# Kernel optimization log

Hardware: AMD Instinct MI355X
Metric: run time of the kernel (lower is better)

Reference implementation:

```python
import jax, jax.numpy as jnp
import numpy as np


def setup_inputs() -> dict:
    key = jax.random.key(0)
    ks = jax.random.split(key, 10)
    N, E, H, T = 50000, 800000, 128, 2
    inp = {
        "hv": jax.random.normal(ks[0], (N, H), jnp.float32),
        "he": jax.random.normal(ks[1], (E, H), jnp.float32),
        "src": jax.random.randint(ks[2], (E,), 0, N, jnp.int32),
        "dst": jax.random.randint(ks[3], (E,), 0, N, jnp.int32),
        "W_msg": jax.random.normal(ks[4], (T, 2 * H, 3 * H), jnp.float32) * 0.05,
        "b_msg": jnp.zeros((T, 2 * H), jnp.float32),
        "W_ih": jax.random.normal(ks[5], (T, 3 * H, 2 * H), jnp.float32) * 0.05,
        "W_hh": jax.random.normal(ks[6], (T, 3 * H, H), jnp.float32) * 0.05,
        "b_ih": jnp.zeros((T, 3 * H), jnp.float32),
        "b_hh": jnp.zeros((T, 3 * H), jnp.float32),
    }
    return inp


def reference(hv, he, src, dst, W_msg, b_msg, W_ih, W_hh, b_ih, b_hh):
    N = hv.shape[0]
    T = W_msg.shape[0]
    # In-degree for mean reduction (DGL mailbox mean). Zero-degree nodes get zero message parts.
    deg = jax.ops.segment_sum(jnp.ones(dst.shape, hv.dtype), dst, num_segments=N)
    safe_deg = jnp.maximum(deg, 1.0)[:, None]  # [N,1]
    # Edge features are constant across rounds -> precompute their per-node mean.
    mean_he = jax.ops.segment_sum(he, dst, num_segments=N) / safe_deg  # [N,H]
    for t in range(T):
        # mean over mailbox of concat([hv_dst, hv_src, he]) then Linear == Linear of means (affine).
        mean_hsrc = jax.ops.segment_sum(hv[src], dst, num_segments=N) / safe_deg  # [N,H]
        x = jnp.concatenate([hv, mean_hsrc, mean_he], axis=1)  # [N,3H]
        a = x @ W_msg[t].T + b_msg[t]  # [N,2H] node activation
        # torch GRUCell(a, hv)
        gi = a @ W_ih[t].T + b_ih[t]   # [N,3H]
        gh = hv @ W_hh[t].T + b_hh[t]  # [N,3H]
        i_r, i_z, i_n = jnp.split(gi, 3, axis=1)
        h_r, h_z, h_n = jnp.split(gh, 3, axis=1)
        r = jax.nn.sigmoid(i_r + h_r)
        z = jax.nn.sigmoid(i_z + h_z)
        n = jnp.tanh(i_n + r * h_n)
        hv = (1.0 - z) * n + z * hv
    return hv
```

## Files before the change

### kernel.cpp

```cpp
#include <hip/hip_runtime.h>
#include <hip/hip_bf16.h>

typedef __bf16 bf16x8 __attribute__((ext_vector_type(8)));
typedef __bf16 bf16x2 __attribute__((ext_vector_type(2)));
typedef float  f32x4  __attribute__((ext_vector_type(4)));

#define MFMA16(a,b,c) __builtin_amdgcn_mfma_f32_16x16x32_bf16((a),(b),(c),0,0,0)

__global__ void k_prepack_weights(const float* __restrict__ wmsg,
                                  const float* __restrict__ wih,
                                  const float* __restrict__ whh,
                                  __bf16* __restrict__ o_msg,
                                  __bf16* __restrict__ o_rz,
                                  __bf16* __restrict__ o_in,
                                  __bf16* __restrict__ o_hn) {
    const int C1 = 2 * 256 * 384;
    const int C2 = C1 + 2 * 256 * 384;
    const int C3 = C2 + 2 * 128 * 256;
    const int C4 = C3 + 2 * 128 * 128;
    int i = blockIdx.x * 256 + threadIdx.x;
    if (i >= C4) return;
    if (i < C1) {
        o_msg[i] = (__bf16)wmsg[i];
    } else if (i < C2) {
        int p = i - C1;
        int t = p / 98304, rem = p % 98304;
        int o = rem / 384, c = rem % 384;
        float v = (c < 128) ? whh[t * 49152 + o * 128 + c]
                            : wih[t * 98304 + o * 256 + (c - 128)];
        o_rz[p] = (__bf16)v;
    } else if (i < C3) {
        int p = i - C2;
        int t = p / 32768, rem = p % 32768;
        int j = rem / 256, k = rem % 256;
        o_in[p] = (__bf16)wih[t * 98304 + (256 + j) * 256 + k];
    } else {
        int p = i - C3;
        int t = p / 16384, rem = p % 16384;
        int j = rem / 128, k = rem % 128;
        o_hn[p] = (__bf16)whh[t * 49152 + (256 + j) * 128 + k];
    }
}

__global__ void k_convert_hv(const float* __restrict__ hv, __bf16* __restrict__ hv_bf,
                             int total8) {
    int i = blockIdx.x * 256 + threadIdx.x;
    if (i >= total8) return;
    const float4* p = (const float4*)(hv + (size_t)i * 8);
    float4 a = p[0], b = p[1];
    bf16x8 o;
    o[0] = (__bf16)a.x; o[1] = (__bf16)a.y; o[2] = (__bf16)a.z; o[3] = (__bf16)a.w;
    o[4] = (__bf16)b.x; o[5] = (__bf16)b.y; o[6] = (__bf16)b.z; o[7] = (__bf16)b.w;
    *(bf16x8*)(hv_bf + (size_t)i * 8) = o;
}

__global__ void k_deg(const int* __restrict__ dst, int* __restrict__ degi, int E) {
    int e = blockIdx.x * 256 + threadIdx.x;
    if (e < E) atomicAdd(&degi[dst[e]], 1);
}

__global__ void k_alloc(const int* __restrict__ degi, int* __restrict__ off,
                        int* __restrict__ cnt, int* __restrict__ counter, int N) {
    int i = blockIdx.x * 256 + threadIdx.x;
    int lane = (int)threadIdx.x & 63;
    int v = (i < N) ? degi[i] : 0;
    int incl = v;
    #pragma unroll
    for (int d = 1; d < 64; d <<= 1) {
        int t = __shfl_up(incl, d, 64);
        if (lane >= d) incl += t;
    }
    int base = 0;
    if (lane == 63) base = atomicAdd(counter, incl);
    base = __shfl(base, 63, 64);
    if (i < N) { off[i] = base + incl - v; cnt[i] = 0; }
}

__global__ void k_bucket(const int* __restrict__ src, const int* __restrict__ dst,
                         const int* __restrict__ off, int* __restrict__ cnt,
                         int2* __restrict__ pairs, int E) {
    int e = blockIdx.x * 256 + threadIdx.x;
    if (e < E) {
        int d = dst[e];
        int p = off[d] + atomicAdd(&cnt[d], 1);
        pairs[p] = make_int2(src[e], e);
    }
}

__global__ void k_gather_both(const __bf16* __restrict__ hv_bf, const float* __restrict__ he,
                              const int2* __restrict__ pairs,
                              const int* __restrict__ off, const int* __restrict__ degi,
                              __bf16* __restrict__ hsrc_mean, __bf16* __restrict__ he_mean,
                              int N) {
    int node = blockIdx.x * 4 + ((int)threadIdx.x >> 6);
    if (node >= N) return;
    int lane = (int)threadIdx.x & 63;
    int beg = off[node], deg = degi[node];
    int end = beg + deg;
    float h0x=0.f,h0y=0.f,h1x=0.f,h1y=0.f,h2x=0.f,h2y=0.f,h3x=0.f,h3y=0.f;
    float e0x=0.f,e0y=0.f,e1x=0.f,e1y=0.f,e2x=0.f,e2y=0.f,e3x=0.f,e3y=0.f;
    int p = beg;
    for (; p + 3 < end; p += 4) {
        int2 a = pairs[p], b = pairs[p+1], c = pairs[p+2], d = pairs[p+3];
        bf16x2 v0 = *(const bf16x2*)(hv_bf + (size_t)a.x * 128 + lane * 2);
        bf16x2 v1 = *(const bf16x2*)(hv_bf + (size_t)b.x * 128 + lane * 2);
        bf16x2 v2 = *(const bf16x2*)(hv_bf + (size_t)c.x * 128 + lane * 2);
        bf16x2 v3 = *(const bf16x2*)(hv_bf + (size_t)d.x * 128 + lane * 2);
        float2 w0 = *(const float2*)(he + (size_t)a.y * 128 + lane * 2);
        float2 w1 = *(const float2*)(he + (size_t)b.y * 128 + lane * 2);
        float2 w2 = *(const float2*)(he + (size_t)c.y * 128 + lane * 2);
        float2 w3 = *(const float2*)(he + (size_t)d.y * 128 + lane * 2);
        h0x += (float)v0[0]; h0y += (float)v0[1]; h1x += (float)v1[0]; h1y += (float)v1[1];
        h2x += (float)v2[0]; h2y += (float)v2[1]; h3x += (float)v3[0]; h3y += (float)v3[1];
        e0x += w0.x; e0y += w0.y; e1x += w1.x; e1y += w1.y;
        e2x += w2.x; e2y += w2.y; e3x += w3.x; e3y += w3.y;
    }
    for (; p < end; ++p) {
        int2 a = pairs[p];
        bf16x2 v0 = *(const bf16x2*)(hv_bf + (size_t)a.x * 128 + lane * 2);
        float2 w0 = *(const float2*)(he + (size_t)a.y * 128 + lane * 2);
        h0x += (float)v0[0]; h0y += (float)v0[1];
        e0x += w0.x; e0y += w0.y;
    }
    float s = 1.0f / fmaxf((float)deg, 1.0f);
    bf16x2 oh; oh[0] = (__bf16)((h0x+h1x+h2x+h3x) * s); oh[1] = (__bf16)((h0y+h1y+h2y+h3y) * s);
    bf16x2 oe; oe[0] = (__bf16)((e0x+e1x+e2x+e3x) * s); oe[1] = (__bf16)((e0y+e1y+e2y+e3y) * s);
    *(bf16x2*)(hsrc_mean + (size_t)node * 128 + lane * 2) = oh;
    *(bf16x2*)(he_mean   + (size_t)node * 128 + lane * 2) = oe;
}

__global__ void k_gather_hv(const __bf16* __restrict__ hv_bf, const int2* __restrict__ pairs,
                            const int* __restrict__ off, const int* __restrict__ degi,
                            __bf16* __restrict__ hsrc_mean, int N) {
    int node = blockIdx.x * 4 + ((int)threadIdx.x >> 6);
    if (node >= N) return;
    int lane = (int)threadIdx.x & 63;
    int beg = off[node], deg = degi[node];
    int end = beg + deg;
    float a0x=0.f,a0y=0.f,a1x=0.f,a1y=0.f,a2x=0.f,a2y=0.f,a3x=0.f,a3y=0.f;
    int p = beg;
    for (; p + 3 < end; p += 4) {
        int2 pa = pairs[p], pb = pairs[p+1], pc = pairs[p+2], pd = pairs[p+3];
        bf16x2 v0 = *(const bf16x2*)(hv_bf + (size_t)pa.x * 128 + lane * 2);
        bf16x2 v1 = *(const bf16x2*)(hv_bf + (size_t)pb.x * 128 + lane * 2);
        bf16x2 v2 = *(const bf16x2*)(hv_bf + (size_t)pc.x * 128 + lane * 2);
        bf16x2 v3 = *(const bf16x2*)(hv_bf + (size_t)pd.x * 128 + lane * 2);
        a0x += (float)v0[0]; a0y += (float)v0[1]; a1x += (float)v1[0]; a1y += (float)v1[1];
        a2x += (float)v2[0]; a2y += (float)v2[1]; a3x += (float)v3[0]; a3y += (float)v3[1];
    }
    for (; p < end; ++p) {
        int2 pa = pairs[p];
        bf16x2 v0 = *(const bf16x2*)(hv_bf + (size_t)pa.x * 128 + lane * 2);
        a0x += (float)v0[0]; a0y += (float)v0[1];
    }
    float s = 1.0f / fmaxf((float)deg, 1.0f);
    bf16x2 o; o[0] = (__bf16)((a0x+a1x+a2x+a3x) * s); o[1] = (__bf16)((a0y+a1y+a2y+a3y) * s);
    *(bf16x2*)(hsrc_mean + (size_t)node * 128 + lane * 2) = o;
}

template<bool WRITE_BF>
__launch_bounds__(256, 4)
__global__ void k_fused_round(
    const float* __restrict__ hv_hold,
    __bf16* __restrict__ hv_bf,
    const __bf16* __restrict__ hsrc_mean,
    const __bf16* __restrict__ he_mean,
    const __bf16* __restrict__ Wmsg,
    const float* __restrict__ bmsg,
    const __bf16* __restrict__ Wrz,
    const __bf16* __restrict__ Win,
    const __bf16* __restrict__ Whn,
    const float* __restrict__ bih,
    const float* __restrict__ bhh,
    float* __restrict__ hv_out, int N)
{
    __shared__ __bf16 xs[32][392];

    const int tid = threadIdx.x;
    const int m0  = blockIdx.x * 32;

    for (int idx = tid; idx < 32 * 48; idx += 256) {
        int row = idx / 48;
        int c   = idx - row * 48;
        int part = c >> 4;
        int c8   = (c & 15) * 8;
        int node = m0 + row;
        const __bf16* base = (part == 0) ? hv_bf : ((part == 1) ? hsrc_mean : he_mean);
        bf16x8 v = {};
        if (node < N) v = *(const bf16x8*)(base + (size_t)node * 128 + c8);
        *(bf16x8*)&xs[row][part * 128 + c8] = v;
    }
    __syncthreads();

    const int wave = tid >> 6;
    const int lane = tid & 63;
    const int lr = lane & 15;
    const int lk = lane >> 4;

    f32x4 acc1[2][4] = {};
    #pragma unroll 2
    for (int k0 = 0; k0 < 384; k0 += 32) {
        bf16x8 a0 = *(const bf16x8*)&xs[lr][k0 + lk * 8];
        bf16x8 a1 = *(const bf16x8*)&xs[16 + lr][k0 + lk * 8];
        #pragma unroll
        for (int c = 0; c < 4; ++c) {
            const __bf16* wp = Wmsg + (size_t)(wave * 64 + c * 16 + lr) * 384 + k0 + lk * 8;
            bf16x8 b = *(const bf16x8*)wp;
            acc1[0][c] = MFMA16(a0, b, acc1[0][c]);
            acc1[1][c] = MFMA16(a1, b, acc1[1][c]);
        }
    }
    __syncthreads();

    f32x4 acchn[2][2] = {};
    {
        #pragma unroll
        for (int k0 = 0; k0 < 128; k0 += 32) {
            bf16x8 a0 = *(const bf16x8*)&xs[lr][k0 + lk * 8];
            bf16x8 a1 = *(const bf16x8*)&xs[16 + lr][k0 + lk * 8];
            #pragma unroll
            for (int q = 0; q < 2; ++q) {
                int o = wave * 32 + q * 16 + lr;
                bf16x8 b = *(const bf16x8*)(Whn + (size_t)o * 128 + k0 + lk * 8);
                acchn[0][q] = MFMA16(a0, b, acchn[0][q]);
                acchn[1][q] = MFMA16(a1, b, acchn[1][q]);
            }
        }
    }

    #pragma unroll
    for (int mf = 0; mf < 2; ++mf) {
        #pragma unroll
        for (int c = 0; c < 4; ++c) {
            int n = wave * 64 + c * 16 + lr;
            float bias = bmsg[n];
            #pragma unroll
            for (int r = 0; r < 4; ++r) {
                int m = mf * 16 + lk * 4 + r;
                xs[m][128 + n] = (__bf16)(acc1[mf][c][r] + bias);
            }
        }
    }
    __syncthreads();

    f32x4 accrz[2][4] = {};
    #pragma unroll 2
    for (int k0 = 0; k0 < 384; k0 += 32) {
        bf16x8 a0 = *(const bf16x8*)&xs[lr][k0 + lk * 8];
        bf16x8 a1 = *(const bf16x8*)&xs[16 + lr][k0 + lk * 8];
        #pragma unroll
        for (int q = 0; q < 4; ++q) {
            int o = (q >> 1) * 128 + wave * 32 + (q & 1) * 16 + lr;
            bf16x8 b = *(const bf16x8*)(Wrz + (size_t)o * 384 + k0 + lk * 8);
            accrz[0][q] = MFMA16(a0, b, accrz[0][q]);
            accrz[1][q] = MFMA16(a1, b, accrz[1][q]);
        }
    }

    f32x4 accin[2][2] = {};
    #pragma unroll 2
    for (int k0 = 0; k0 < 256; k0 += 32) {
        bf16x8 a0 = *(const bf16x8*)&xs[lr][128 + k0 + lk * 8];
        bf16x8 a1 = *(const bf16x8*)&xs[16 + lr][128 + k0 + lk * 8];
        #pragma unroll
        for (int q = 0; q < 2; ++q) {
            int o = wave * 32 + q * 16 + lr;
            bf16x8 b = *(const bf16x8*)(Win + (size_t)o * 256 + k0 + lk * 8);
            accin[0][q] = MFMA16(a0, b, accin[0][q]);
            accin[1][q] = MFMA16(a1, b, accin[1][q]);
        }
    }

    #pragma unroll
    for (int mf = 0; mf < 2; ++mf) {
        #pragma unroll
        for (int j = 0; j < 2; ++j) {
            int hcol = wave * 32 + j * 16 + lr;
            float brz_r = bih[hcol]       + bhh[hcol];
            float brz_z = bih[128 + hcol] + bhh[128 + hcol];
            float b_in  = bih[256 + hcol];
            float b_hn  = bhh[256 + hcol];
            #pragma unroll
            for (int r = 0; r < 4; ++r) {
                int m = mf * 16 + lk * 4 + r;
                int node = m0 + m;
                if (node < N) {
                    float rg = 1.f / (1.f + __expf(-(accrz[mf][0 + j][r] + brz_r)));
                    float zg = 1.f / (1.f + __expf(-(accrz[mf][2 + j][r] + brz_z)));
                    float ng = tanhf(accin[mf][j][r] + b_in + rg * (acchn[mf][j][r] + b_hn));
                    float hold = hv_hold[(size_t)node * 128 + hcol];
                    float hnew = (1.f - zg) * ng + zg * hold;
                    hv_out[(size_t)node * 128 + hcol] = hnew;
                    if (WRITE_BF) hv_bf[(size_t)node * 128 + hcol] = (__bf16)hnew;
                }
            }
        }
    }
}

extern "C" void kernel_launch(void* const* d_in, const int* in_sizes, int n_in,
                              void* d_out, int out_size, void* d_ws, size_t ws_size,
                              hipStream_t stream)
{
    const float* hv   = (const float*)d_in[0];
    const float* he   = (const float*)d_in[1];
    const int*   src  = (const int*)d_in[2];
    const int*   dst  = (const int*)d_in[3];
    const float* Wmsg = (const float*)d_in[4];
    const float* bmsg = (const float*)d_in[5];
    const float* Wih  = (const float*)d_in[6];
    const float* Whh  = (const float*)d_in[7];
    const float* bih  = (const float*)d_in[8];
    const float* bhh  = (const float*)d_in[9];

    const int H = 128;
    const int N = in_sizes[0] / H;
    const int E = in_sizes[2];

    char* w = (char*)d_ws;
    __bf16* he_mean   = (__bf16*)w;  w += (size_t)N * H * 2;
    __bf16* hsrc_mean = (__bf16*)w;  w += (size_t)N * H * 2;
    __bf16* hv_bf     = (__bf16*)w;  w += (size_t)N * H * 2;
    int* degi    = (int*)w;  w += (size_t)N * 4;
    int* counter = (int*)w;  w += 4;
    int* off     = (int*)w;  w += (size_t)N * 4;
    int* cnt     = (int*)w;  w += (size_t)N * 4;
    w = (char*)(((uintptr_t)w + 15) & ~(uintptr_t)15);
    int2* pairs  = (int2*)w; w += (size_t)E * 8;
    __bf16* wmsg_bf = (__bf16*)w;
    __bf16* wrz_bf  = wmsg_bf + 2 * 256 * 384;
    __bf16* win_bf  = wrz_bf  + 2 * 256 * 384;
    __bf16* whn_bf  = win_bf  + 2 * 128 * 256;

    hipMemsetAsync(degi, 0, ((size_t)N + 1) * 4, stream);

    const int prepack_total = 2*256*384 + 2*256*384 + 2*128*256 + 2*128*128;
    k_prepack_weights<<<(prepack_total + 255) / 256, 256, 0, stream>>>(
        Wmsg, Wih, Whh, wmsg_bf, wrz_bf, win_bf, whn_bf);
    k_convert_hv<<<(N * H / 8 + 255) / 256, 256, 0, stream>>>(hv, hv_bf, N * H / 8);

    k_deg<<<(E + 255) / 256, 256, 0, stream>>>(dst, degi, E);
    k_alloc<<<(N + 255) / 256, 256, 0, stream>>>(degi, off, cnt, counter, N);
    k_bucket<<<(E + 255) / 256, 256, 0, stream>>>(src, dst, off, cnt, pairs, E);

    float* out = (float*)d_out;

    k_gather_both<<<(N + 3) / 4, 256, 0, stream>>>(hv_bf, he, pairs, off, degi,
                                                   hsrc_mean, he_mean, N);
    k_fused_round<true><<<(N + 31) / 32, 256, 0, stream>>>(
        hv, hv_bf, hsrc_mean, he_mean,
        wmsg_bf, bmsg,
        wrz_bf, win_bf, whn_bf,
        bih, bhh, out, N);

    k_gather_hv<<<(N + 3) / 4, 256, 0, stream>>>(hv_bf, pairs, off, degi, hsrc_mean, N);
    k_fused_round<false><<<(N + 31) / 32, 256, 0, stream>>>(
        out, hv_bf, hsrc_mean, he_mean,
        wmsg_bf + (size_t)256 * 384, bmsg + 256,
        wrz_bf + (size_t)256 * 384, win_bf + (size_t)128 * 256, whn_bf + (size_t)128 * 128,
        bih + 384, bhh + 384, out, N);
}
```

Measured before the change: 505.2 us.

## Fuse neighbor gather into GRU round kernels and merge setup kernels

The per-node mean gathers (hv over src, and he in round one) move into the fused GEMM/GRU kernel, which writes the means straight into shared memory instead of a global intermediate. hv's bf16 copy is double-buffered so round one can write the new state while other blocks still read the old one. Weight prepack, hv conversion and degree counting merge into one launch to cut launch overhead. The trade-off is that each 32-node block now does irregular gather latency before its MFMA work, which may hurt occupancy and overlap compared with separate kernels.

```diff
diff --git a/kernel.cpp b/kernel.cpp
--- a/kernel.cpp
+++ b/kernel.cpp
@@ -7,56 +7,54 @@
 
 #define MFMA16(a,b,c) __builtin_amdgcn_mfma_f32_16x16x32_bf16((a),(b),(c),0,0,0)
 
-__global__ void k_prepack_weights(const float* __restrict__ wmsg,
-                                  const float* __restrict__ wih,
-                                  const float* __restrict__ whh,
-                                  __bf16* __restrict__ o_msg,
-                                  __bf16* __restrict__ o_rz,
-                                  __bf16* __restrict__ o_in,
-                                  __bf16* __restrict__ o_hn) {
+__global__ void k_setup(const float* __restrict__ wmsg, const float* __restrict__ wih,
+                        const float* __restrict__ whh, const float* __restrict__ hv,
+                        const int* __restrict__ dst,
+                        __bf16* __restrict__ o_msg, __bf16* __restrict__ o_rz,
+                        __bf16* __restrict__ o_in, __bf16* __restrict__ o_hn,
+                        __bf16* __restrict__ hv_bf, int* __restrict__ degi,
+                        int nb_pre, int nb_hv, int hv8, int E) {
     const int C1 = 2 * 256 * 384;
     const int C2 = C1 + 2 * 256 * 384;
     const int C3 = C2 + 2 * 128 * 256;
     const int C4 = C3 + 2 * 128 * 128;
-    int i = blockIdx.x * 256 + threadIdx.x;
-    if (i >= C4) return;
-    if (i < C1) {
-        o_msg[i] = (__bf16)wmsg[i];
-    } else if (i < C2) {
-        int p = i - C1;
-        int t = p / 98304, rem = p % 98304;
-        int o = rem / 384, c = rem % 384;
-        float v = (c < 128) ? whh[t * 49152 + o * 128 + c]
-                            : wih[t * 98304 + o * 256 + (c - 128)];
-        o_rz[p] = (__bf16)v;
-    } else if (i < C3) {
-        int p = i - C2;
-        int t = p / 32768, rem = p % 32768;
-        int j = rem / 256, k = rem % 256;
-        o_in[p] = (__bf16)wih[t * 98304 + (256 + j) * 256 + k];
+    int b = blockIdx.x;
+    if (b < nb_pre) {
+        int i = b * 256 + threadIdx.x;
+        if (i >= C4) return;
+        if (i < C1) {
+            o_msg[i] = (__bf16)wmsg[i];
+        } else if (i < C2) {
+            int p = i - C1;
+            int t = p / 98304, rem = p % 98304;
+            int o = rem / 384, c = rem % 384;
+            float v = (c < 128) ? whh[t * 49152 + o * 128 + c]
+                                : wih[t * 98304 + o * 256 + (c - 128)];
+            o_rz[p] = (__bf16)v;
+        } else if (i < C3) {
+            int p = i - C2;
+            int t = p / 32768, rem = p % 32768;
+            int j = rem / 256, k = rem % 256;
+            o_in[p] = (__bf16)wih[t * 98304 + (256 + j) * 256 + k];
+        } else {
+            int p = i - C3;
+            int t = p / 16384, rem = p % 16384;
+            int j = rem / 128, k = rem % 128;
+            o_hn[p] = (__bf16)whh[t * 49152 + (256 + j) * 128 + k];
+        }
+    } else if (b < nb_pre + nb_hv) {
+        int i = (b - nb_pre) * 256 + threadIdx.x;
+        if (i >= hv8) return;
+        const float4* p = (const float4*)(hv + (size_t)i * 8);
+        float4 a = p[0], c = p[1];
+        bf16x8 o;
+        o[0] = (__bf16)a.x; o[1] = (__bf16)a.y; o[2] = (__bf16)a.z; o[3] = (__bf16)a.w;
+        o[4] = (__bf16)c.x; o[5] = (__bf16)c.y; o[6] = (__bf16)c.z; o[7] = (__bf16)c.w;
+        *(bf16x8*)(hv_bf + (size_t)i * 8) = o;
     } else {
-        int p = i - C3;
-        int t = p / 16384, rem = p % 16384;
-        int j = rem / 128, k = rem % 128;
-        o_hn[p] = (__bf16)whh[t * 49152 + (256 + j) * 128 + k];
-    }
-}
-
-__global__ void k_convert_hv(const float* __restrict__ hv, __bf16* __restrict__ hv_bf,
-                             int total8) {
-    int i = blockIdx.x * 256 + threadIdx.x;
-    if (i >= total8) return;
-    const float4* p = (const float4*)(hv + (size_t)i * 8);
-    float4 a = p[0], b = p[1];
-    bf16x8 o;
-    o[0] = (__bf16)a.x; o[1] = (__bf16)a.y; o[2] = (__bf16)a.z; o[3] = (__bf16)a.w;
-    o[4] = (__bf16)b.x; o[5] = (__bf16)b.y; o[6] = (__bf16)b.z; o[7] = (__bf16)b.w;
-    *(bf16x8*)(hv_bf + (size_t)i * 8) = o;
-}
-
-__global__ void k_deg(const int* __restrict__ dst, int* __restrict__ degi, int E) {
-    int e = blockIdx.x * 256 + threadIdx.x;
-    if (e < E) atomicAdd(&degi[dst[e]], 1);
+        int e = (b - nb_pre - nb_hv) * 256 + threadIdx.x;
+        if (e < E) atomicAdd(&degi[dst[e]], 1);
+    }
 }
 
 __global__ void k_alloc(const int* __restrict__ degi, int* __restrict__ off,
@@ -87,84 +85,16 @@
     }
 }
 
-__global__ void k_gather_both(const __bf16* __restrict__ hv_bf, const float* __restrict__ he,
-                              const int2* __restrict__ pairs,
-                              const int* __restrict__ off, const int* __restrict__ degi,
-                              __bf16* __restrict__ hsrc_mean, __bf16* __restrict__ he_mean,
-                              int N) {
-    int node = blockIdx.x * 4 + ((int)threadIdx.x >> 6);
-    if (node >= N) return;
-    int lane = (int)threadIdx.x & 63;
-    int beg = off[node], deg = degi[node];
-    int end = beg + deg;
-    float h0x=0.f,h0y=0.f,h1x=0.f,h1y=0.f,h2x=0.f,h2y=0.f,h3x=0.f,h3y=0.f;
-    float e0x=0.f,e0y=0.f,e1x=0.f,e1y=0.f,e2x=0.f,e2y=0.f,e3x=0.f,e3y=0.f;
-    int p = beg;
-    for (; p + 3 < end; p += 4) {
-        int2 a = pairs[p], b = pairs[p+1], c = pairs[p+2], d = pairs[p+3];
-        bf16x2 v0 = *(const bf16x2*)(hv_bf + (size_t)a.x * 128 + lane * 2);
-        bf16x2 v1 = *(const bf16x2*)(hv_bf + (size_t)b.x * 128 + lane * 2);
-        bf16x2 v2 = *(const bf16x2*)(hv_bf + (size_t)c.x * 128 + lane * 2);
-        bf16x2 v3 = *(const bf16x2*)(hv_bf + (size_t)d.x * 128 + lane * 2);
-        float2 w0 = *(const float2*)(he + (size_t)a.y * 128 + lane * 2);
-        float2 w1 = *(const float2*)(he + (size_t)b.y * 128 + lane * 2);
-        float2 w2 = *(const float2*)(he + (size_t)c.y * 128 + lane * 2);
-        float2 w3 = *(const float2*)(he + (size_t)d.y * 128 + lane * 2);
-        h0x += (float)v0[0]; h0y += (float)v0[1]; h1x += (float)v1[0]; h1y += (float)v1[1];
-        h2x += (float)v2[0]; h2y += (float)v2[1]; h3x += (float)v3[0]; h3y += (float)v3[1];
-        e0x += w0.x; e0y += w0.y; e1x += w1.x; e1y += w1.y;
-        e2x += w2.x; e2y += w2.y; e3x += w3.x; e3y += w3.y;
-    }
-    for (; p < end; ++p) {
-        int2 a = pairs[p];
-        bf16x2 v0 = *(const bf16x2*)(hv_bf + (size_t)a.x * 128 + lane * 2);
-        float2 w0 = *(const float2*)(he + (size_t)a.y * 128 + lane * 2);
-        h0x += (float)v0[0]; h0y += (float)v0[1];
-        e0x += w0.x; e0y += w0.y;
-    }
-    float s = 1.0f / fmaxf((float)deg, 1.0f);
-    bf16x2 oh; oh[0] = (__bf16)((h0x+h1x+h2x+h3x) * s); oh[1] = (__bf16)((h0y+h1y+h2y+h3y) * s);
-    bf16x2 oe; oe[0] = (__bf16)((e0x+e1x+e2x+e3x) * s); oe[1] = (__bf16)((e0y+e1y+e2y+e3y) * s);
-    *(bf16x2*)(hsrc_mean + (size_t)node * 128 + lane * 2) = oh;
-    *(bf16x2*)(he_mean   + (size_t)node * 128 + lane * 2) = oe;
-}
-
-__global__ void k_gather_hv(const __bf16* __restrict__ hv_bf, const int2* __restrict__ pairs,
-                            const int* __restrict__ off, const int* __restrict__ degi,
-                            __bf16* __restrict__ hsrc_mean, int N) {
-    int node = blockIdx.x * 4 + ((int)threadIdx.x >> 6);
-    if (node >= N) return;
-    int lane = (int)threadIdx.x & 63;
-    int beg = off[node], deg = degi[node];
-    int end = beg + deg;
-    float a0x=0.f,a0y=0.f,a1x=0.f,a1y=0.f,a2x=0.f,a2y=0.f,a3x=0.f,a3y=0.f;
-    int p = beg;
-    for (; p + 3 < end; p += 4) {
-        int2 pa = pairs[p], pb = pairs[p+1], pc = pairs[p+2], pd = pairs[p+3];
-        bf16x2 v0 = *(const bf16x2*)(hv_bf + (size_t)pa.x * 128 + lane * 2);
-        bf16x2 v1 = *(const bf16x2*)(hv_bf + (size_t)pb.x * 128 + lane * 2);
-        bf16x2 v2 = *(const bf16x2*)(hv_bf + (size_t)pc.x * 128 + lane * 2);
-        bf16x2 v3 = *(const bf16x2*)(hv_bf + (size_t)pd.x * 128 + lane * 2);
-        a0x += (float)v0[0]; a0y += (float)v0[1]; a1x += (float)v1[0]; a1y += (float)v1[1];
-        a2x += (float)v2[0]; a2y += (float)v2[1]; a3x += (float)v3[0]; a3y += (float)v3[1];
-    }
-    for (; p < end; ++p) {
-        int2 pa = pairs[p];
-        bf16x2 v0 = *(const bf16x2*)(hv_bf + (size_t)pa.x * 128 + lane * 2);
-        a0x += (float)v0[0]; a0y += (float)v0[1];
-    }
-    float s = 1.0f / fmaxf((float)deg, 1.0f);
-    bf16x2 o; o[0] = (__bf16)((a0x+a1x+a2x+a3x) * s); o[1] = (__bf16)((a0y+a1y+a2y+a3y) * s);
-    *(bf16x2*)(hsrc_mean + (size_t)node * 128 + lane * 2) = o;
-}
-
-template<bool WRITE_BF>
+template<int ROUND>
 __launch_bounds__(256, 4)
-__global__ void k_fused_round(
+__global__ void k_fused(
     const float* __restrict__ hv_hold,
-    __bf16* __restrict__ hv_bf,
-    const __bf16* __restrict__ hsrc_mean,
-    const __bf16* __restrict__ he_mean,
+    const __bf16* __restrict__ hv_rd,
+    __bf16* __restrict__ hv_wr,
+    const float* __restrict__ he,
+    __bf16* __restrict__ he_mean_g,
+    const int2* __restrict__ pairs,
+    const int* __restrict__ off, const int* __restrict__ degi,
     const __bf16* __restrict__ Wmsg,
     const float* __restrict__ bmsg,
     const __bf16* __restrict__ Wrz,
@@ -176,24 +106,83 @@
 {
     __shared__ __bf16 xs[32][392];
 
-    const int tid = threadIdx.x;
-    const int m0  = blockIdx.x * 32;
-
-    for (int idx = tid; idx < 32 * 48; idx += 256) {
-        int row = idx / 48;
-        int c   = idx - row * 48;
-        int part = c >> 4;
-        int c8   = (c & 15) * 8;
-        int node = m0 + row;
-        const __bf16* base = (part == 0) ? hv_bf : ((part == 1) ? hsrc_mean : he_mean);
-        bf16x8 v = {};
-        if (node < N) v = *(const bf16x8*)(base + (size_t)node * 128 + c8);
-        *(bf16x8*)&xs[row][part * 128 + c8] = v;
-    }
-    __syncthreads();
-
+    const int tid  = threadIdx.x;
+    const int m0   = blockIdx.x * 32;
     const int wave = tid >> 6;
     const int lane = tid & 63;
+
+    for (int idx = tid; idx < 32 * 16; idx += 256) {
+        int row = idx >> 4, c8 = (idx & 15) * 8;
+        int node = m0 + row;
+        bf16x8 v = {};
+        if (node < N) v = *(const bf16x8*)(hv_rd + (size_t)node * 128 + c8);
+        *(bf16x8*)&xs[row][c8] = v;
+    }
+    if (ROUND == 2) {
+        for (int idx = tid; idx < 32 * 16; idx += 256) {
+            int row = idx >> 4, c8 = (idx & 15) * 8;
+            int node = m0 + row;
+            bf16x8 v = {};
+            if (node < N) v = *(const bf16x8*)(he_mean_g + (size_t)node * 128 + c8);
+            *(bf16x8*)&xs[row][256 + c8] = v;
+        }
+    }
+
+    for (int s = 0; s < 8; ++s) {
+        int row  = wave * 8 + s;
+        int node = m0 + row;
+        if (node < N) {
+            int beg = off[node], deg = degi[node];
+            int end = beg + deg;
+            float h0x=0.f,h0y=0.f,h1x=0.f,h1y=0.f,h2x=0.f,h2y=0.f,h3x=0.f,h3y=0.f;
+            float e0x=0.f,e0y=0.f,e1x=0.f,e1y=0.f,e2x=0.f,e2y=0.f,e3x=0.f,e3y=0.f;
+            int p = beg;
+            for (; p + 3 < end; p += 4) {
+                int2 a = pairs[p], b = pairs[p+1], c = pairs[p+2], d = pairs[p+3];
+                bf16x2 v0 = *(const bf16x2*)(hv_rd + (size_t)a.x * 128 + lane * 2);
+                bf16x2 v1 = *(const bf16x2*)(hv_rd + (size_t)b.x * 128 + lane * 2);
+                bf16x2 v2 = *(const bf16x2*)(hv_rd + (size_t)c.x * 128 + lane * 2);
+                bf16x2 v3 = *(const bf16x2*)(hv_rd + (size_t)d.x * 128 + lane * 2);
+                h0x += (float)v0[0]; h0y += (float)v0[1];
+                h1x += (float)v1[0]; h1y += (float)v1[1];
+                h2x += (float)v2[0]; h2y += (float)v2[1];
+                h3x += (float)v3[0]; h3y += (float)v3[1];
+                if (ROUND == 1) {
+                    float2 w0 = *(const float2*)(he + (size_t)a.y * 128 + lane * 2);
+                    float2 w1 = *(const float2*)(he + (size_t)b.y * 128 + lane * 2);
+                    float2 w2 = *(const float2*)(he + (size_t)c.y * 128 + lane * 2);
+                    float2 w3 = *(const float2*)(he + (size_t)d.y * 128 + lane * 2);
+                    e0x += w0.x; e0y += w0.y; e1x += w1.x; e1y += w1.y;
+                    e2x += w2.x; e2y += w2.y; e3x += w3.x; e3y += w3.y;
+                }
+            }
+            for (; p < end; ++p) {
+                int2 a = pairs[p];
+                bf16x2 v0 = *(const bf16x2*)(hv_rd + (size_t)a.x * 128 + lane * 2);
+                h0x += (float)v0[0]; h0y += (float)v0[1];
+                if (ROUND == 1) {
+                    float2 w0 = *(const float2*)(he + (size_t)a.y * 128 + lane * 2);
+                    e0x += w0.x; e0y += w0.y;
+                }
+            }
+            float sc = 1.0f / fmaxf((float)deg, 1.0f);
+            bf16x2 oh; oh[0] = (__bf16)((h0x+h1x+h2x+h3x) * sc);
+            oh[1] = (__bf16)((h0y+h1y+h2y+h3y) * sc);
+            *(bf16x2*)&xs[row][128 + lane * 2] = oh;
+            if (ROUND == 1) {
+                bf16x2 oe; oe[0] = (__bf16)((e0x+e1x+e2x+e3x) * sc);
+                oe[1] = (__bf16)((e0y+e1y+e2y+e3y) * sc);
+                *(bf16x2*)&xs[row][256 + lane * 2] = oe;
+                *(bf16x2*)(he_mean_g + (size_t)node * 128 + lane * 2) = oe;
+            }
+        } else {
+            bf16x2 z = {};
+            *(bf16x2*)&xs[row][128 + lane * 2] = z;
+            if (ROUND == 1) *(bf16x2*)&xs[row][256 + lane * 2] = z;
+        }
+    }
+    __syncthreads();
+
     const int lr = lane & 15;
     const int lk = lane >> 4;
 
@@ -213,18 +202,16 @@
     __syncthreads();
 
     f32x4 acchn[2][2] = {};
-    {
-        #pragma unroll
-        for (int k0 = 0; k0 < 128; k0 += 32) {
-            bf16x8 a0 = *(const bf16x8*)&xs[lr][k0 + lk * 8];
-            bf16x8 a1 = *(const bf16x8*)&xs[16 + lr][k0 + lk * 8];
-            #pragma unroll
-            for (int q = 0; q < 2; ++q) {
-                int o = wave * 32 + q * 16 + lr;
-                bf16x8 b = *(const bf16x8*)(Whn + (size_t)o * 128 + k0 + lk * 8);
-                acchn[0][q] = MFMA16(a0, b, acchn[0][q]);
-                acchn[1][q] = MFMA16(a1, b, acchn[1][q]);
-            }
+    #pragma unroll
+    for (int k0 = 0; k0 < 128; k0 += 32) {
+        bf16x8 a0 = *(const bf16x8*)&xs[lr][k0 + lk * 8];
+        bf16x8 a1 = *(const bf16x8*)&xs[16 + lr][k0 + lk * 8];
+        #pragma unroll
+        for (int q = 0; q < 2; ++q) {
+            int o = wave * 32 + q * 16 + lr;
+            bf16x8 b = *(const bf16x8*)(Whn + (size_t)o * 128 + k0 + lk * 8);
+            acchn[0][q] = MFMA16(a0, b, acchn[0][q]);
+            acchn[1][q] = MFMA16(a1, b, acchn[1][q]);
         }
     }
 
@@ -291,7 +278,7 @@
                     float hold = hv_hold[(size_t)node * 128 + hcol];
                     float hnew = (1.f - zg) * ng + zg * hold;
                     hv_out[(size_t)node * 128 + hcol] = hnew;
-                    if (WRITE_BF) hv_bf[(size_t)node * 128 + hcol] = (__bf16)hnew;
+                    if (ROUND == 1) hv_wr[(size_t)node * 128 + hcol] = (__bf16)hnew;
                 }
             }
         }
@@ -318,9 +305,9 @@
     const int E = in_sizes[2];
 
     char* w = (char*)d_ws;
-    __bf16* he_mean   = (__bf16*)w;  w += (size_t)N * H * 2;
-    __bf16* hsrc_mean = (__bf16*)w;  w += (size_t)N * H * 2;
-    __bf16* hv_bf     = (__bf16*)w;  w += (size_t)N * H * 2;
+    __bf16* he_mean = (__bf16*)w;  w += (size_t)N * H * 2;
+    __bf16* hv_bfA  = (__bf16*)w;  w += (size_t)N * H * 2;
+    __bf16* hv_bfB  = (__bf16*)w;  w += (size_t)N * H * 2;
     int* degi    = (int*)w;  w += (size_t)N * 4;
     int* counter = (int*)w;  w += 4;
     int* off     = (int*)w;  w += (size_t)N * 4;
@@ -335,27 +322,27 @@
     hipMemsetAsync(degi, 0, ((size_t)N + 1) * 4, stream);
 
     const int prepack_total = 2*256*384 + 2*256*384 + 2*128*256 + 2*128*128;
-    k_prepack_weights<<<(prepack_total + 255) / 256, 256, 0, stream>>>(
-        Wmsg, Wih, Whh, wmsg_bf, wrz_bf, win_bf, whn_bf);
-    k_convert_hv<<<(N * H / 8 + 255) / 256, 256, 0, stream>>>(hv, hv_bf, N * H / 8);
-
-    k_deg<<<(E + 255) / 256, 256, 0, stream>>>(dst, degi, E);
+    const int hv8    = N * H / 8;
+    const int nb_pre = (prepack_total + 255) / 256;
+    const int nb_hv  = (hv8 + 255) / 256;
+    const int nb_deg = (E + 255) / 256;
+    k_setup<<<nb_pre + nb_hv + nb_deg, 256, 0, stream>>>(
+        Wmsg, Wih, Whh, hv, dst,
+        wmsg_bf, wrz_bf, win_bf, whn_bf, hv_bfA, degi,
+        nb_pre, nb_hv, hv8, E);
+
     k_alloc<<<(N + 255) / 256, 256, 0, stream>>>(degi, off, cnt, counter, N);
     k_bucket<<<(E + 255) / 256, 256, 0, stream>>>(src, dst, off, cnt, pairs, E);
 
     float* out = (float*)d_out;
-
-    k_gather_both<<<(N + 3) / 4, 256, 0, stream>>>(hv_bf, he, pairs, off, degi,
-                                                   hsrc_mean, he_mean, N);
-    k_fused_round<true><<<(N + 31) / 32, 256, 0, stream>>>(
-        hv, hv_bf, hsrc_mean, he_mean,
-        wmsg_bf, bmsg,
-        wrz_bf, win_bf, whn_bf,
-        bih, bhh, out, N);
-
-    k_gather_hv<<<(N + 3) / 4, 256, 0, stream>>>(hv_bf, pairs, off, degi, hsrc_mean, N);
-    k_fused_round<false><<<(N + 31) / 32, 256, 0, stream>>>(
-        out, hv_bf, hsrc_mean, he_mean,
+    const int nb_f = (N + 31) / 32;
+
+    k_fused<1><<<nb_f, 256, 0, stream>>>(
+        hv, hv_bfA, hv_bfB, he, he_mean, pairs, off, degi,
+        wmsg_bf, bmsg, wrz_bf, win_bf, whn_bf, bih, bhh, out, N);
+
+    k_fused<2><<<nb_f, 256, 0, stream>>>(
+        out, hv_bfB, nullptr, nullptr, he_mean, pairs, off, degi,
         wmsg_bf + (size_t)256 * 384, bmsg + 256,
         wrz_bf + (size_t)256 * 384, win_bf + (size_t)128 * 256, whn_bf + (size_t)128 * 128,
         bih + 384, bhh + 384, out, N);
```

After: 544.5 us. 1.08x slower.

## Double fused-round row tile to 64 and merge setup kernels into one launch

Applied to the files above, without the earlier changes.

The fused GRU round kernel now processes 64 nodes per block instead of 32, so each weight fragment loaded from global memory feeds four MFMAs instead of two. This halves the weight traffic per node and halves the block count. In exchange it doubles LDS and accumulator registers, and launch bounds drop to 2 blocks per SM. Separately, the weight prepack, hv bf16 conversion and degree-count kernels are merged into one launch that dispatches on block index, removing two launches.

```diff
diff --git a/kernel.cpp b/kernel.cpp
--- a/kernel.cpp
+++ b/kernel.cpp
@@ -7,56 +7,54 @@
 
 #define MFMA16(a,b,c) __builtin_amdgcn_mfma_f32_16x16x32_bf16((a),(b),(c),0,0,0)
 
-__global__ void k_prepack_weights(const float* __restrict__ wmsg,
-                                  const float* __restrict__ wih,
-                                  const float* __restrict__ whh,
-                                  __bf16* __restrict__ o_msg,
-                                  __bf16* __restrict__ o_rz,
-                                  __bf16* __restrict__ o_in,
-                                  __bf16* __restrict__ o_hn) {
+__global__ void k_setup(const float* __restrict__ wmsg, const float* __restrict__ wih,
+                        const float* __restrict__ whh, const float* __restrict__ hv,
+                        const int* __restrict__ dst,
+                        __bf16* __restrict__ o_msg, __bf16* __restrict__ o_rz,
+                        __bf16* __restrict__ o_in, __bf16* __restrict__ o_hn,
+                        __bf16* __restrict__ hv_bf, int* __restrict__ degi,
+                        int nb_pre, int nb_hv, int hv8, int E) {
     const int C1 = 2 * 256 * 384;
     const int C2 = C1 + 2 * 256 * 384;
     const int C3 = C2 + 2 * 128 * 256;
     const int C4 = C3 + 2 * 128 * 128;
-    int i = blockIdx.x * 256 + threadIdx.x;
-    if (i >= C4) return;
-    if (i < C1) {
-        o_msg[i] = (__bf16)wmsg[i];
-    } else if (i < C2) {
-        int p = i - C1;
-        int t = p / 98304, rem = p % 98304;
-        int o = rem / 384, c = rem % 384;
-        float v = (c < 128) ? whh[t * 49152 + o * 128 + c]
-                            : wih[t * 98304 + o * 256 + (c - 128)];
-        o_rz[p] = (__bf16)v;
-    } else if (i < C3) {
-        int p = i - C2;
-        int t = p / 32768, rem = p % 32768;
-        int j = rem / 256, k = rem % 256;
-        o_in[p] = (__bf16)wih[t * 98304 + (256 + j) * 256 + k];
+    int b = blockIdx.x;
+    if (b < nb_pre) {
+        int i = b * 256 + threadIdx.x;
+        if (i >= C4) return;
+        if (i < C1) {
+            o_msg[i] = (__bf16)wmsg[i];
+        } else if (i < C2) {
+            int p = i - C1;
+            int t = p / 98304, rem = p % 98304;
+            int o = rem / 384, c = rem % 384;
+            float v = (c < 128) ? whh[t * 49152 + o * 128 + c]
+                                : wih[t * 98304 + o * 256 + (c - 128)];
+            o_rz[p] = (__bf16)v;
+        } else if (i < C3) {
+            int p = i - C2;
+            int t = p / 32768, rem = p % 32768;
+            int j = rem / 256, k = rem % 256;
+            o_in[p] = (__bf16)wih[t * 98304 + (256 + j) * 256 + k];
+        } else {
+            int p = i - C3;
+            int t = p / 16384, rem = p % 16384;
+            int j = rem / 128, k = rem % 128;
+            o_hn[p] = (__bf16)whh[t * 49152 + (256 + j) * 128 + k];
+        }
+    } else if (b < nb_pre + nb_hv) {
+        int i = (b - nb_pre) * 256 + threadIdx.x;
+        if (i >= hv8) return;
+        const float4* p = (const float4*)(hv + (size_t)i * 8);
+        float4 a = p[0], c = p[1];
+        bf16x8 o;
+        o[0] = (__bf16)a.x; o[1] = (__bf16)a.y; o[2] = (__bf16)a.z; o[3] = (__bf16)a.w;
+        o[4] = (__bf16)c.x; o[5] = (__bf16)c.y; o[6] = (__bf16)c.z; o[7] = (__bf16)c.w;
+        *(bf16x8*)(hv_bf + (size_t)i * 8) = o;
     } else {
-        int p = i - C3;
-        int t = p / 16384, rem = p % 16384;
-        int j = rem / 128, k = rem % 128;
-        o_hn[p] = (__bf16)whh[t * 49152 + (256 + j) * 128 + k];
-    }
-}
-
-__global__ void k_convert_hv(const float* __restrict__ hv, __bf16* __restrict__ hv_bf,
-                             int total8) {
-    int i = blockIdx.x * 256 + threadIdx.x;
-    if (i >= total8) return;
-    const float4* p = (const float4*)(hv + (size_t)i * 8);
-    float4 a = p[0], b = p[1];
-    bf16x8 o;
-    o[0] = (__bf16)a.x; o[1] = (__bf16)a.y; o[2] = (__bf16)a.z; o[3] = (__bf16)a.w;
-    o[4] = (__bf16)b.x; o[5] = (__bf16)b.y; o[6] = (__bf16)b.z; o[7] = (__bf16)b.w;
-    *(bf16x8*)(hv_bf + (size_t)i * 8) = o;
-}
-
-__global__ void k_deg(const int* __restrict__ dst, int* __restrict__ degi, int E) {
-    int e = blockIdx.x * 256 + threadIdx.x;
-    if (e < E) atomicAdd(&degi[dst[e]], 1);
+        int e = (b - nb_pre - nb_hv) * 256 + threadIdx.x;
+        if (e < E) atomicAdd(&degi[dst[e]], 1);
+    }
 }
 
 __global__ void k_alloc(const int* __restrict__ degi, int* __restrict__ off,
@@ -159,7 +157,7 @@
 }
 
 template<bool WRITE_BF>
-__launch_bounds__(256, 4)
+__launch_bounds__(256, 2)
 __global__ void k_fused_round(
     const float* __restrict__ hv_hold,
     __bf16* __restrict__ hv_bf,
@@ -174,12 +172,12 @@
     const float* __restrict__ bhh,
     float* __restrict__ hv_out, int N)
 {
-    __shared__ __bf16 xs[32][392];
+    __shared__ __bf16 xs[64][392];
 
     const int tid = threadIdx.x;
-    const int m0  = blockIdx.x * 32;
-
-    for (int idx = tid; idx < 32 * 48; idx += 256) {
+    const int m0  = blockIdx.x * 64;
+
+    for (int idx = tid; idx < 64 * 48; idx += 256) {
         int row = idx / 48;
         int c   = idx - row * 48;
         int part = c >> 4;
@@ -197,39 +195,44 @@
     const int lr = lane & 15;
     const int lk = lane >> 4;
 
-    f32x4 acc1[2][4] = {};
+    f32x4 acc1[4][4] = {};
     #pragma unroll 2
     for (int k0 = 0; k0 < 384; k0 += 32) {
         bf16x8 a0 = *(const bf16x8*)&xs[lr][k0 + lk * 8];
         bf16x8 a1 = *(const bf16x8*)&xs[16 + lr][k0 + lk * 8];
+        bf16x8 a2 = *(const bf16x8*)&xs[32 + lr][k0 + lk * 8];
+        bf16x8 a3 = *(const bf16x8*)&xs[48 + lr][k0 + lk * 8];
         #pragma unroll
         for (int c = 0; c < 4; ++c) {
-            const __bf16* wp = Wmsg + (size_t)(wave * 64 + c * 16 + lr) * 384 + k0 + lk * 8;
-            bf16x8 b = *(const bf16x8*)wp;
+            bf16x8 b = *(const bf16x8*)(Wmsg + (size_t)(wave * 64 + c * 16 + lr) * 384 + k0 + lk * 8);
             acc1[0][c] = MFMA16(a0, b, acc1[0][c]);
             acc1[1][c] = MFMA16(a1, b, acc1[1][c]);
+            acc1[2][c] = MFMA16(a2, b, acc1[2][c]);
+            acc1[3][c] = MFMA16(a3, b, acc1[3][c]);
         }
     }
     __syncthreads();
 
-    f32x4 acchn[2][2] = {};
-    {
-        #pragma unroll
-        for (int k0 = 0; k0 < 128; k0 += 32) {
-            bf16x8 a0 = *(const bf16x8*)&xs[lr][k0 + lk * 8];
-            bf16x8 a1 = *(const bf16x8*)&xs[16 + lr][k0 + lk * 8];
-            #pragma unroll
-            for (int q = 0; q < 2; ++q) {
-                int o = wave * 32 + q * 16 + lr;
-                bf16x8 b = *(const bf16x8*)(Whn + (size_t)o * 128 + k0 + lk * 8);
-                acchn[0][q] = MFMA16(a0, b, acchn[0][q]);
-                acchn[1][q] = MFMA16(a1, b, acchn[1][q]);
-            }
-        }
-    }
-
+    f32x4 acchn[4][2] = {};
     #pragma unroll
-    for (int mf = 0; mf < 2; ++mf) {
+    for (int k0 = 0; k0 < 128; k0 += 32) {
+        bf16x8 a0 = *(const bf16x8*)&xs[lr][k0 + lk * 8];
+        bf16x8 a1 = *(const bf16x8*)&xs[16 + lr][k0 + lk * 8];
+        bf16x8 a2 = *(const bf16x8*)&xs[32 + lr][k0 + lk * 8];
+        bf16x8 a3 = *(const bf16x8*)&xs[48 + lr][k0 + lk * 8];
+        #pragma unroll
+        for (int j = 0; j < 2; ++j) {
+            int o = wave * 32 + j * 16 + lr;
+            bf16x8 b = *(const bf16x8*)(Whn + (size_t)o * 128 + k0 + lk * 8);
+            acchn[0][j] = MFMA16(a0, b, acchn[0][j]);
+            acchn[1][j] = MFMA16(a1, b, acchn[1][j]);
+            acchn[2][j] = MFMA16(a2, b, acchn[2][j]);
+            acchn[3][j] = MFMA16(a3, b, acchn[3][j]);
+        }
+    }
+
+    #pragma unroll
+    for (int mf = 0; mf < 4; ++mf) {
         #pragma unroll
         for (int c = 0; c < 4; ++c) {
             int n = wave * 64 + c * 16 + lr;
@@ -243,36 +246,44 @@
     }
     __syncthreads();
 
-    f32x4 accrz[2][4] = {};
+    f32x4 accrz[4][4] = {};
     #pragma unroll 2
     for (int k0 = 0; k0 < 384; k0 += 32) {
         bf16x8 a0 = *(const bf16x8*)&xs[lr][k0 + lk * 8];
         bf16x8 a1 = *(const bf16x8*)&xs[16 + lr][k0 + lk * 8];
+        bf16x8 a2 = *(const bf16x8*)&xs[32 + lr][k0 + lk * 8];
+        bf16x8 a3 = *(const bf16x8*)&xs[48 + lr][k0 + lk * 8];
         #pragma unroll
         for (int q = 0; q < 4; ++q) {
             int o = (q >> 1) * 128 + wave * 32 + (q & 1) * 16 + lr;
             bf16x8 b = *(const bf16x8*)(Wrz + (size_t)o * 384 + k0 + lk * 8);
             accrz[0][q] = MFMA16(a0, b, accrz[0][q]);
             accrz[1][q] = MFMA16(a1, b, accrz[1][q]);
-        }
-    }
-
-    f32x4 accin[2][2] = {};
+            accrz[2][q] = MFMA16(a2, b, accrz[2][q]);
+            accrz[3][q] = MFMA16(a3, b, accrz[3][q]);
+        }
+    }
+
+    f32x4 accin[4][2] = {};
     #pragma unroll 2
     for (int k0 = 0; k0 < 256; k0 += 32) {
         bf16x8 a0 = *(const bf16x8*)&xs[lr][128 + k0 + lk * 8];
         bf16x8 a1 = *(const bf16x8*)&xs[16 + lr][128 + k0 + lk * 8];
-        #pragma unroll
-        for (int q = 0; q < 2; ++q) {
-            int o = wave * 32 + q * 16 + lr;
+        bf16x8 a2 = *(const bf16x8*)&xs[32 + lr][128 + k0 + lk * 8];
+        bf16x8 a3 = *(const bf16x8*)&xs[48 + lr][128 + k0 + lk * 8];
+        #pragma unroll
+        for (int j = 0; j < 2; ++j) {
+            int o = wave * 32 + j * 16 + lr;
             bf16x8 b = *(const bf16x8*)(Win + (size_t)o * 256 + k0 + lk * 8);
-            accin[0][q] = MFMA16(a0, b, accin[0][q]);
-            accin[1][q] = MFMA16(a1, b, accin[1][q]);
+            accin[0][j] = MFMA16(a0, b, accin[0][j]);
+            accin[1][j] = MFMA16(a1, b, accin[1][j]);
+            accin[2][j] = MFMA16(a2, b, accin[2][j]);
+            accin[3][j] = MFMA16(a3, b, accin[3][j]);
         }
     }
 
     #pragma unroll
-    for (int mf = 0; mf < 2; ++mf) {
+    for (int mf = 0; mf < 4; ++mf) {
         #pragma unroll
         for (int j = 0; j < 2; ++j) {
             int hcol = wave * 32 + j * 16 + lr;
@@ -335,26 +346,29 @@
     hipMemsetAsync(degi, 0, ((size_t)N + 1) * 4, stream);
 
     const int prepack_total = 2*256*384 + 2*256*384 + 2*128*256 + 2*128*128;
-    k_prepack_weights<<<(prepack_total + 255) / 256, 256, 0, stream>>>(
-        Wmsg, Wih, Whh, wmsg_bf, wrz_bf, win_bf, whn_bf);
-    k_convert_hv<<<(N * H / 8 + 255) / 256, 256, 0, stream>>>(hv, hv_bf, N * H / 8);
-
-    k_deg<<<(E + 255) / 256, 256, 0, stream>>>(dst, degi, E);
+    const int hv8    = N * H / 8;
+    const int nb_pre = (prepack_total + 255) / 256;
+    const int nb_hv  = (hv8 + 255) / 256;
+    const int nb_deg = (E + 255) / 256;
+    k_setup<<<nb_pre + nb_hv + nb_deg, 256, 0, stream>>>(
+        Wmsg, Wih, Whh, hv, dst,
+        wmsg_bf, wrz_bf, win_bf, whn_bf, hv_bf, degi,
+        nb_pre, nb_hv, hv8, E);
+
     k_alloc<<<(N + 255) / 256, 256, 0, stream>>>(degi, off, cnt, counter, N);
     k_bucket<<<(E + 255) / 256, 256, 0, stream>>>(src, dst, off, cnt, pairs, E);
 
     float* out = (float*)d_out;
+    const int nb_f = (N + 63) / 64;
 
     k_gather_both<<<(N + 3) / 4, 256, 0, stream>>>(hv_bf, he, pairs, off, degi,
                                                    hsrc_mean, he_mean, N);
-    k_fused_round<true><<<(N + 31) / 32, 256, 0, stream>>>(
+    k_fused_round<true><<<nb_f, 256, 0, stream>>>(
         hv, hv_bf, hsrc_mean, he_mean,
-        wmsg_bf, bmsg,
-        wrz_bf, win_bf, whn_bf,
-        bih, bhh, out, N);
+        wmsg_bf, bmsg, wrz_bf, win_bf, whn_bf, bih, bhh, out, N);
 
     k_gather_hv<<<(N + 3) / 4, 256, 0, stream>>>(hv_bf, pairs, off, degi, hsrc_mean, N);
-    k_fused_round<false><<<(N + 31) / 32, 256, 0, stream>>>(
+    k_fused_round<false><<<nb_f, 256, 0, stream>>>(
         out, hv_bf, hsrc_mean, he_mean,
         wmsg_bf + (size_t)256 * 384, bmsg + 256,
         wrz_bf + (size_t)256 * 384, win_bf + (size_t)128 * 256, whn_bf + (size_t)128 * 128,
```

New measurement: 462.8 us. -8.4%, faster.
